# Kernel tuning notes

Measured on AMD Instinct MI355X. Metric: run time of the kernel, lower is better.

## Reference

```python
import jax, jax.numpy as jnp
import numpy as np

LOG2 = 0.6931471805599453

def ssp(x):
    # ShiftedSoftplus: softplus(x) - log(2)
    return jax.nn.softplus(x) - jnp.asarray(LOG2, x.dtype)

def setup_inputs() -> dict:
    key = jax.random.key(0)
    ks = jax.random.split(key, 12)
    B, N, D, F, R, P = 1, 50000, 128, 128, 20, 1600000
    s = lambda fan_in: 1.0 / np.sqrt(fan_in)
    return {
        "x": jax.random.normal(ks[0], (B, N, D), jnp.float32),
        "f_ij": jax.random.uniform(ks[1], (P, R), jnp.float32),
        "idx_i": jax.random.randint(ks[2], (P,), 0, B * N),
        "idx_j": jax.random.randint(ks[3], (P,), 0, B * N),
        "rcut_ij": jax.random.uniform(ks[4], (P,), jnp.float32),
        "W_in": jax.random.uniform(ks[5], (F, D), jnp.float32, -s(D), s(D)),
        "b_in": jax.random.uniform(ks[6], (F,), jnp.float32, -s(D), s(D)),
        "W_filter": jax.random.uniform(ks[7], (F, R), jnp.float32, -s(R), s(R)),
        "b_filter": jax.random.uniform(ks[8], (F,), jnp.float32, -s(R), s(R)),
        "W_out": jax.random.uniform(ks[9], (D, F), jnp.float32, -s(F), s(F)),
        "b_out": jax.random.uniform(ks[10], (D,), jnp.float32, -s(F), s(F)),
    }

def reference(x, f_ij, idx_i, idx_j, rcut_ij, W_in, b_in, W_filter, b_filter, W_out, b_out):
    B, N, _ = x.shape
    # input_to_feature: Linear(nr_atom_basis -> nr_filters)
    h = jnp.einsum('bnd,fd->bnf', x, W_in) + b_in          # [B,N,F]
    h = h.reshape(B * N, -1)                                # [B*N,F]
    # filter network: Linear(nr_rbf -> nr_filters) + ShiftedSoftplus, scaled by cutoff
    Wij = ssp(jnp.einsum('pr,fr->pf', f_ij, W_filter) + b_filter) * rcut_ij[:, None]  # [P,F]
    # gather -> mul -> scatter_add
    x_ij = h[idx_j] * Wij                                   # [P,F]
    agg = jax.ops.segment_sum(x_ij, idx_i, num_segments=B * N)  # [B*N,F]
    # feature_to_output: Linear(nr_filters -> nr_atom_basis) + ShiftedSoftplus
    out = ssp(jnp.einsum('nf,df->nd', agg, W_out) + b_out)  # [B*N,D]
    return out.reshape(B, N, 128)
```

## Files before the change

kernel.cpp:

```cpp
#include <hip/hip_runtime.h>
#include <hip/hip_bf16.h>

static constexpr float kLog2 = 0.6931471805599453f;

__device__ __forceinline__ float sspf(float x) {
    return fmaxf(x, 0.0f) + __logf(1.0f + __expf(-fabsf(x))) - kLog2;
}

typedef __attribute__((ext_vector_type(8))) _Float16 half8;
typedef __attribute__((ext_vector_type(4))) _Float16 half4v;
typedef __attribute__((ext_vector_type(4))) float float4v;

__device__ __forceinline__ int hperm(int n) {
    return ((n >> 6) << 6) | (((n >> 5) & 1) << 5) | (((n >> 2) & 3) << 3) |
           (((n >> 4) & 1) << 2) | (n & 3);
}

template <bool PERM, bool ACT, typename OUT>
__device__ __forceinline__ void gemm_mfma_body(const float* __restrict__ A,
                                               const float* __restrict__ B,
                                               const float* __restrict__ bias,
                                               OUT* __restrict__ C, int M,
                                               int blockid) {
    constexpr int LDH = 136;
    __shared__ _Float16 Als[64 * LDH];
    __shared__ _Float16 Bls[128 * LDH];
    const int tid = threadIdx.x;
    const int rowbase = blockid * 64;
#pragma unroll
    for (int j = 0; j < 8; ++j) {
        int idx = j * 256 + tid;
        int r = idx >> 5, c4 = (idx & 31) << 2;
        int rg = rowbase + r;
        rg = rg < M ? rg : (M - 1);
        float4 v = *(const float4*)(A + (size_t)rg * 128 + c4);
        half4v hv = {(_Float16)v.x, (_Float16)v.y, (_Float16)v.z, (_Float16)v.w};
        *(half4v*)&Als[r * LDH + c4] = hv;
    }
#pragma unroll
    for (int j = 0; j < 16; ++j) {
        int idx = j * 256 + tid;
        int r = idx >> 5, c4 = (idx & 31) << 2;
        float4 v = *(const float4*)(B + (size_t)r * 128 + c4);
        half4v hv = {(_Float16)v.x, (_Float16)v.y, (_Float16)v.z, (_Float16)v.w};
        *(half4v*)&Bls[r * LDH + c4] = hv;
    }
    __syncthreads();

    const int wave = tid >> 6, lane = tid & 63;
    const int l15 = lane & 15, q = lane >> 4;
    float4v acc[8];
#pragma unroll
    for (int nt = 0; nt < 8; ++nt) acc[nt] = (float4v){0.f, 0.f, 0.f, 0.f};
    const int am = wave * 16 + l15;
#pragma unroll
    for (int kk = 0; kk < 4; ++kk) {
        half8 af = *(const half8*)&Als[am * LDH + kk * 32 + q * 8];
#pragma unroll
        for (int nt = 0; nt < 8; ++nt) {
            half8 bfv = *(const half8*)&Bls[(nt * 16 + l15) * LDH + kk * 32 + q * 8];
            acc[nt] = __builtin_amdgcn_mfma_f32_16x16x32_f16(af, bfv, acc[nt], 0, 0, 0);
        }
    }
#pragma unroll
    for (int nt = 0; nt < 8; ++nt) {
        int n = nt * 16 + l15;
        float bv = bias[n];
        const int pn = PERM ? hperm(n) : n;
#pragma unroll
        for (int r = 0; r < 4; ++r) {
            int m = rowbase + wave * 16 + q * 4 + r;
            if (m < M) {
                float v = acc[nt][r] + bv;
                if (ACT) v = sspf(v);
                C[(size_t)m * 128 + pn] = (OUT)v;
            }
        }
    }
}

__global__ __launch_bounds__(256) void gemm_in_count_kernel(
    const float* __restrict__ A, const float* __restrict__ B,
    const float* __restrict__ bias, _Float16* __restrict__ C, int M,
    const int* __restrict__ idx_i, int* __restrict__ counts, int P,
    int gemm_blocks) {
    if ((int)blockIdx.x < gemm_blocks) {
        gemm_mfma_body<true, false, _Float16>(A, B, bias, C, M, blockIdx.x);
    } else {
        const int nthr = (gridDim.x - gemm_blocks) * 256;
        for (int p = (blockIdx.x - gemm_blocks) * 256 + threadIdx.x; p < P;
             p += nthr)
            atomicAdd(&counts[idx_i[p]], 1);
    }
}

__global__ __launch_bounds__(256) void gemm_out_kernel(
    const float* __restrict__ A, const float* __restrict__ B,
    const float* __restrict__ bias, float* __restrict__ C, int M) {
    gemm_mfma_body<false, true, float>(A, B, bias, C, M, blockIdx.x);
}

__global__ __launch_bounds__(256) void alloc_starts_kernel(
    const int* __restrict__ counts, int* __restrict__ starts,
    int* __restrict__ cursor, int* __restrict__ gtot, int N) {
    __shared__ int s[256];
    __shared__ int base;
    const int t = threadIdx.x, g = blockIdx.x * 256 + t;
    const int c = g < N ? counts[g] : 0;
    s[t] = c;
    __syncthreads();
    for (int o = 1; o < 256; o <<= 1) {
        int v = t >= o ? s[t - o] : 0;
        __syncthreads();
        s[t] += v;
        __syncthreads();
    }
    if (t == 255) base = atomicAdd(gtot, s[255]);
    __syncthreads();
    const int excl = base + s[t] - c;
    if (g < N) {
        starts[g] = excl;
        cursor[g] = excl;
    }
}

__global__ __launch_bounds__(256) void fill16_kernel(
    const int* __restrict__ idx_i, const int* __restrict__ idx_j,
    const float* __restrict__ rcut, int* __restrict__ cursor,
    int4* __restrict__ meta, int P) {
    int p = blockIdx.x * 256 + threadIdx.x;
    if (p >= P) return;
    const int pos = atomicAdd(&cursor[idx_i[p]], 1);
    meta[pos] = make_int4(idx_j[p] << 7, __float_as_int(rcut[p]), p, 0);
}

__global__ __launch_bounds__(256) void gather_direct_kernel(
    const int4* __restrict__ meta, const float* __restrict__ f_ij,
    const float* __restrict__ Wf, const float* __restrict__ bf,
    const _Float16* __restrict__ h16, const int* __restrict__ starts,
    const int* __restrict__ counts, float* __restrict__ agg, int N) {
    const int lane = threadIdx.x & 63;
    const int gwave = (blockIdx.x * 256 + threadIdx.x) >> 6;
    const int nwaves = (gridDim.x * 256) >> 6;
    const int l15 = lane & 15, q = lane >> 4;
    const int fh = gwave & 1;
    const int fbase = fh * 64;

    half8 wfr[4];
#pragma unroll
    for (int t = 0; t < 4; ++t) {
        const int n = fbase + t * 16 + l15;
        const float* wr = Wf + (size_t)n * 20;
        float v[8];
#pragma unroll
        for (int j = 0; j < 8; ++j) {
            int k = q * 8 + j;
            v[j] = (k < 20) ? wr[k] : ((k == 20) ? bf[n] : 0.0f);
        }
        wfr[t] = (half8){(_Float16)v[0], (_Float16)v[1], (_Float16)v[2],
                         (_Float16)v[3], (_Float16)v[4], (_Float16)v[5],
                         (_Float16)v[6], (_Float16)v[7]};
    }
    const float4v zero = {0.f, 0.f, 0.f, 0.f};
    const _Float16* hws = h16 + fbase + q * 8;

    for (int u = gwave; u < 2 * N; u += nwaves) {
        const int i = u >> 1;
        const int s = __builtin_amdgcn_readfirstlane(starts[i]);
        const int cnt = __builtin_amdgcn_readfirstlane(counts[i]);
        const int e = s + cnt;
        float4v acc[4];
#pragma unroll
        for (int t = 0; t < 4; ++t) acc[t] = zero;

        if (cnt > 0) {
            int4 mt_c = meta[min(s + l15, e - 1)];
            int4 mt_n = (s + 16 < e) ? meta[min(s + 16 + l15, e - 1)] : mt_c;
            float4 fa_c = {0, 0, 0, 0}, fb_c = {0, 0, 0, 0};
            float4 fa_p = {0, 0, 0, 0}, fb_p = {0, 0, 0, 0};
            {
                const float* fp = f_ij + (size_t)mt_c.z * 20;
                if (q <= 2) fa_c = *(const float4*)(fp + q * 8);
                if (q <= 1) fb_c = *(const float4*)(fp + q * 8 + 4);
                const float* fp2 = f_ij + (size_t)mt_n.z * 20;
                if (q <= 2) fa_p = *(const float4*)(fp2 + q * 8);
                if (q <= 1) fb_p = *(const float4*)(fp2 + q * 8 + 4);
            }

            for (int c0 = s; c0 < e; c0 += 16) {
                const _Float16* hp = hws + mt_c.x;
                half8 hv0 = *(const half8*)hp;
                half8 hv1 = *(const half8*)(hp + 32);
                int4 mt_n2 = mt_n;
                if (c0 + 32 < e) mt_n2 = meta[min(c0 + 32 + l15, e - 1)];
                float b0 = 0.f, b1 = 0.f, b2 = 0.f, b3 = 0.f;
                float b4 = 0.f, b5 = 0.f, b6 = 0.f, b7 = 0.f;
                if (q <= 2) { b0 = fa_c.x; b1 = fa_c.y; b2 = fa_c.z; b3 = fa_c.w; }
                if (q <= 1) { b4 = fb_c.x; b5 = fb_c.y; b6 = fb_c.z; b7 = fb_c.w; }
                if (q == 2) b4 = 1.0f;
                const half8 bfc = (half8){(_Float16)b0, (_Float16)b1, (_Float16)b2,
                                          (_Float16)b3, (_Float16)b4, (_Float16)b5,
                                          (_Float16)b6, (_Float16)b7};
                const float rc = (c0 + l15 < e) ? __int_as_float(mt_c.y) : 0.0f;
#pragma unroll
                for (int t = 0; t < 4; ++t) {
                    float4v d = __builtin_amdgcn_mfma_f32_16x16x32_f16(
                        wfr[t], bfc, zero, 0, 0, 0);
                    const half8& hv = (t < 2) ? hv0 : hv1;
                    const int hb = (t & 1) * 4;
#pragma unroll
                    for (int r = 0; r < 4; ++r) {
                        float w = sspf(d[r]) * rc;
                        acc[t][r] = fmaf(w, (float)hv[hb + r], acc[t][r]);
                    }
                }
                mt_c = mt_n; mt_n = mt_n2;
                fa_c = fa_p; fb_c = fb_p;
                if (c0 + 32 < e) {
                    const float* fp = f_ij + (size_t)mt_n.z * 20;
                    if (q <= 2) fa_p = *(const float4*)(fp + q * 8);
                    if (q <= 1) fb_p = *(const float4*)(fp + q * 8 + 4);
                }
            }
        }
#pragma unroll
        for (int m = 1; m <= 8; m <<= 1)
#pragma unroll
            for (int t = 0; t < 4; ++t)
#pragma unroll
                for (int r = 0; r < 4; ++r)
                    acc[t][r] += __shfl_xor(acc[t][r], m, 64);
        if (l15 == 0) {
#pragma unroll
            for (int t = 0; t < 4; ++t) {
                float4 o = {acc[t][0], acc[t][1], acc[t][2], acc[t][3]};
                *(float4*)(agg + (size_t)i * 128 + fbase + t * 16 + q * 4) = o;
            }
        }
    }
}

extern "C" void kernel_launch(void* const* d_in, const int* in_sizes, int n_in,
                              void* d_out, int out_size, void* d_ws, size_t ws_size,
                              hipStream_t stream) {
    const float* x     = (const float*)d_in[0];
    const float* f_ij  = (const float*)d_in[1];
    const int*   idx_i = (const int*)d_in[2];
    const int*   idx_j = (const int*)d_in[3];
    const float* rcut  = (const float*)d_in[4];
    const float* W_in  = (const float*)d_in[5];
    const float* b_in  = (const float*)d_in[6];
    const float* W_f   = (const float*)d_in[7];
    const float* b_f   = (const float*)d_in[8];
    const float* W_out = (const float*)d_in[9];
    const float* b_out = (const float*)d_in[10];

    const int N = in_sizes[0] / 128;
    const int P = in_sizes[2];

    char* ws = (char*)d_ws;
    size_t off = 0;
    auto alloc = [&](size_t bytes) {
        void* ptr = ws + off;
        off += (bytes + 15) & ~(size_t)15;
        return ptr;
    };
    int* counts  = (int*)alloc((size_t)N * 4 + 16);
    int* gtot    = counts + N;
    int* starts  = (int*)alloc((size_t)N * 4);
    int* cursor  = (int*)alloc((size_t)N * 4);
    _Float16* h16 = (_Float16*)alloc((size_t)N * 128 * 2);
    int4* meta   = (int4*)alloc((size_t)P * 16);

    float* agg = (float*)d_out;

    const int mblocks = (N + 63) / 64;
    const int cblocks = 768;
    const int NB = (N + 255) / 256;

    hipMemsetAsync(counts, 0, (size_t)N * 4 + 16, stream);
    gemm_in_count_kernel<<<mblocks + cblocks, 256, 0, stream>>>(
        x, W_in, b_in, h16, N, idx_i, counts, P, mblocks);
    alloc_starts_kernel<<<NB, 256, 0, stream>>>(counts, starts, cursor, gtot, N);
    fill16_kernel<<<(P + 255) / 256, 256, 0, stream>>>(
        idx_i, idx_j, rcut, cursor, meta, P);
    gather_direct_kernel<<<4096, 256, 0, stream>>>(
        meta, f_ij, W_f, b_f, h16, starts, counts, agg, N);
    gemm_out_kernel<<<mblocks, 256, 0, stream>>>(agg, W_out, b_out, (float*)d_out, N);
}
```

Before: 677.1 us.

## Pack fp16 f_ij rows with pair metadata into sorted 48-byte records

The fill kernel now reads each f_ij row once, in order, converts it to fp16 and writes it with rcut and idx_j into a 48-byte record at the sorted position. The gather kernel then reads these contiguous records instead of chasing a pair index into f_ij. It also software-pipelines the h16 row loads one chunk ahead, using shuffles to broadcast rcut and the neighbour offset. This trades a larger intermediate buffer and more write traffic in the fill pass for coalesced, indirection-free reads in the gather loop.

New measurement: 614.8 us. -9.2%, faster.

```diff
diff --git a/kernel.cpp b/kernel.cpp
--- a/kernel.cpp
+++ b/kernel.cpp
@@ -124,21 +124,41 @@
     }
 }
 
-__global__ __launch_bounds__(256) void fill16_kernel(
+__global__ __launch_bounds__(256) void fill48_kernel(
     const int* __restrict__ idx_i, const int* __restrict__ idx_j,
-    const float* __restrict__ rcut, int* __restrict__ cursor,
-    int4* __restrict__ meta, int P) {
+    const float* __restrict__ rcut, const float* __restrict__ f_ij,
+    int* __restrict__ cursor, char* __restrict__ rec, int P) {
     int p = blockIdx.x * 256 + threadIdx.x;
     if (p >= P) return;
     const int pos = atomicAdd(&cursor[idx_i[p]], 1);
-    meta[pos] = make_int4(idx_j[p] << 7, __float_as_int(rcut[p]), p, 0);
-}
-
-__global__ __launch_bounds__(256) void gather_direct_kernel(
-    const int4* __restrict__ meta, const float* __restrict__ f_ij,
-    const float* __restrict__ Wf, const float* __restrict__ bf,
-    const _Float16* __restrict__ h16, const int* __restrict__ starts,
-    const int* __restrict__ counts, float* __restrict__ agg, int N) {
+    const float* fr = f_ij + (size_t)p * 20;
+    float4 v0 = *(const float4*)(fr + 0);
+    float4 v1 = *(const float4*)(fr + 4);
+    float4 v2 = *(const float4*)(fr + 8);
+    float4 v3 = *(const float4*)(fr + 12);
+    float4 v4 = *(const float4*)(fr + 16);
+    half8 h0 = {(_Float16)v0.x, (_Float16)v0.y, (_Float16)v0.z, (_Float16)v0.w,
+                (_Float16)v1.x, (_Float16)v1.y, (_Float16)v1.z, (_Float16)v1.w};
+    half8 h1 = {(_Float16)v2.x, (_Float16)v2.y, (_Float16)v2.z, (_Float16)v2.w,
+                (_Float16)v3.x, (_Float16)v3.y, (_Float16)v3.z, (_Float16)v3.w};
+    _Float16 t4[4] = {(_Float16)v4.x, (_Float16)v4.y, (_Float16)v4.z,
+                      (_Float16)v4.w};
+    int4 r2;
+    r2.x = *(const int*)&t4[0];
+    r2.y = *(const int*)&t4[2];
+    r2.z = __float_as_int(rcut[p]);
+    r2.w = idx_j[p] << 7;
+    char* dst = rec + (size_t)pos * 48;
+    *(half8*)dst = h0;
+    *(half8*)(dst + 16) = h1;
+    *(int4*)(dst + 32) = r2;
+}
+
+__global__ __launch_bounds__(256) void gather_rec_kernel(
+    const char* __restrict__ rec, const float* __restrict__ Wf,
+    const float* __restrict__ bf, const _Float16* __restrict__ h16,
+    const int* __restrict__ starts, const int* __restrict__ counts,
+    float* __restrict__ agg, int N) {
     const int lane = threadIdx.x & 63;
     const int gwave = (blockIdx.x * 256 + threadIdx.x) >> 6;
     const int nwaves = (gridDim.x * 256) >> 6;
@@ -174,53 +194,61 @@
         for (int t = 0; t < 4; ++t) acc[t] = zero;
 
         if (cnt > 0) {
-            int4 mt_c = meta[min(s + l15, e - 1)];
-            int4 mt_n = (s + 16 < e) ? meta[min(s + 16 + l15, e - 1)] : mt_c;
-            float4 fa_c = {0, 0, 0, 0}, fb_c = {0, 0, 0, 0};
-            float4 fa_p = {0, 0, 0, 0}, fb_p = {0, 0, 0, 0};
+            int4 r_c = {0, 0, 0, 0}, r_n = {0, 0, 0, 0};
             {
-                const float* fp = f_ij + (size_t)mt_c.z * 20;
-                if (q <= 2) fa_c = *(const float4*)(fp + q * 8);
-                if (q <= 1) fb_c = *(const float4*)(fp + q * 8 + 4);
-                const float* fp2 = f_ij + (size_t)mt_n.z * 20;
-                if (q <= 2) fa_p = *(const float4*)(fp2 + q * 8);
-                if (q <= 1) fb_p = *(const float4*)(fp2 + q * 8 + 4);
-            }
+                int pos0 = min(s + l15, e - 1);
+                if (q < 3) r_c = *(const int4*)(rec + (size_t)pos0 * 48 + q * 16);
+            }
+            if (s + 16 < e) {
+                int pos1 = min(s + 16 + l15, e - 1);
+                if (q < 3) r_n = *(const int4*)(rec + (size_t)pos1 * 48 + q * 16);
+            } else {
+                r_n = r_c;
+            }
+            float rcv_c = __int_as_float(__shfl(r_c.z, 32 + l15, 64));
+            int jb_c = __shfl(r_c.w, 32 + l15, 64);
+            const _Float16* hp = hws + jb_c;
+            half8 hv0_c = *(const half8*)hp;
+            half8 hv1_c = *(const half8*)(hp + 32);
 
             for (int c0 = s; c0 < e; c0 += 16) {
-                const _Float16* hp = hws + mt_c.x;
-                half8 hv0 = *(const half8*)hp;
-                half8 hv1 = *(const half8*)(hp + 32);
-                int4 mt_n2 = mt_n;
-                if (c0 + 32 < e) mt_n2 = meta[min(c0 + 32 + l15, e - 1)];
-                float b0 = 0.f, b1 = 0.f, b2 = 0.f, b3 = 0.f;
-                float b4 = 0.f, b5 = 0.f, b6 = 0.f, b7 = 0.f;
-                if (q <= 2) { b0 = fa_c.x; b1 = fa_c.y; b2 = fa_c.z; b3 = fa_c.w; }
-                if (q <= 1) { b4 = fb_c.x; b5 = fb_c.y; b6 = fb_c.z; b7 = fb_c.w; }
-                if (q == 2) b4 = 1.0f;
-                const half8 bfc = (half8){(_Float16)b0, (_Float16)b1, (_Float16)b2,
-                                          (_Float16)b3, (_Float16)b4, (_Float16)b5,
-                                          (_Float16)b6, (_Float16)b7};
-                const float rc = (c0 + l15 < e) ? __int_as_float(mt_c.y) : 0.0f;
+                float rcv_n = __int_as_float(__shfl(r_n.z, 32 + l15, 64));
+                int jb_n = __shfl(r_n.w, 32 + l15, 64);
+                half8 hv0_n = hv0_c, hv1_n = hv1_c;
+                if (c0 + 16 < e) {
+                    const _Float16* hp2 = hws + jb_n;
+                    hv0_n = *(const half8*)hp2;
+                    hv1_n = *(const half8*)(hp2 + 32);
+                }
+                int4 r_n2 = r_n;
+                if (c0 + 32 < e) {
+                    int pos2 = min(c0 + 32 + l15, e - 1);
+                    if (q < 3)
+                        r_n2 = *(const int4*)(rec + (size_t)pos2 * 48 + q * 16);
+                }
+                half8 bfc = *(half8*)&r_c;
+                if (q == 2) {
+                    bfc[4] = (_Float16)1.0f;
+                    bfc[5] = (_Float16)0.0f;
+                    bfc[6] = (_Float16)0.0f;
+                    bfc[7] = (_Float16)0.0f;
+                }
+                const float rcm = (c0 + l15 < e) ? rcv_c : 0.0f;
 #pragma unroll
                 for (int t = 0; t < 4; ++t) {
                     float4v d = __builtin_amdgcn_mfma_f32_16x16x32_f16(
                         wfr[t], bfc, zero, 0, 0, 0);
-                    const half8& hv = (t < 2) ? hv0 : hv1;
+                    const half8& hv = (t < 2) ? hv0_c : hv1_c;
                     const int hb = (t & 1) * 4;
 #pragma unroll
                     for (int r = 0; r < 4; ++r) {
-                        float w = sspf(d[r]) * rc;
+                        float w = sspf(d[r]) * rcm;
                         acc[t][r] = fmaf(w, (float)hv[hb + r], acc[t][r]);
                     }
                 }
-                mt_c = mt_n; mt_n = mt_n2;
-                fa_c = fa_p; fb_c = fb_p;
-                if (c0 + 32 < e) {
-                    const float* fp = f_ij + (size_t)mt_n.z * 20;
-                    if (q <= 2) fa_p = *(const float4*)(fp + q * 8);
-                    if (q <= 1) fb_p = *(const float4*)(fp + q * 8 + 4);
-                }
+                r_c = r_n; r_n = r_n2;
+                rcv_c = rcv_n;
+                hv0_c = hv0_n; hv1_c = hv1_n;
             }
         }
 #pragma unroll
@@ -270,7 +298,7 @@
     int* starts  = (int*)alloc((size_t)N * 4);
     int* cursor  = (int*)alloc((size_t)N * 4);
     _Float16* h16 = (_Float16*)alloc((size_t)N * 128 * 2);
-    int4* meta   = (int4*)alloc((size_t)P * 16);
+    char* rec    = (char*)alloc((size_t)P * 48 + 64);
 
     float* agg = (float*)d_out;
 
@@ -282,9 +310,9 @@
     gemm_in_count_kernel<<<mblocks + cblocks, 256, 0, stream>>>(
         x, W_in, b_in, h16, N, idx_i, counts, P, mblocks);
     alloc_starts_kernel<<<NB, 256, 0, stream>>>(counts, starts, cursor, gtot, N);
-    fill16_kernel<<<(P + 255) / 256, 256, 0, stream>>>(
-        idx_i, idx_j, rcut, cursor, meta, P);
-    gather_direct_kernel<<<4096, 256, 0, stream>>>(
-        meta, f_ij, W_f, b_f, h16, starts, counts, agg, N);
+    fill48_kernel<<<(P + 255) / 256, 256, 0, stream>>>(
+        idx_i, idx_j, rcut, f_ij, cursor, rec, P);
+    gather_rec_kernel<<<4096, 256, 0, stream>>>(
+        rec, W_f, b_f, h16, starts, counts, agg, N);
     gemm_out_kernel<<<mblocks, 256, 0, stream>>>(agg, W_out, b_out, (float*)d_out, N);
 }
```
